# Kernel tuning notes

Measured on AMD Instinct MI355X. Metric: run time of the kernel, lower is better.

The kernel has to match this reference:

```python
import jax, jax.numpy as jnp
import numpy as np

LMBDA = 0.01
GAMMA = 0.5  # resolvant_gamma


def get_mask(evals_x, evals_y, gamma):
    # Standard DPFM resolvant mask, vectorized over batch.
    # evals_x, evals_y: [B, K] nonnegative eigenvalues.
    scale = jnp.maximum(evals_x.max(-1), evals_y.max(-1))[:, None]  # per-batch scaling
    e1 = (evals_x / scale) ** gamma  # [B, K] -> columns of D
    e2 = (evals_y / scale) ** gamma  # [B, K] -> rows of D
    denom = e1[:, None, :] ** 2 + e2[:, :, None] ** 2  # [B, K, K]
    M_re = (e2[:, :, None] - e1[:, None, :]) / denom
    M_im = 1.0 / denom
    return M_re ** 2 + M_im ** 2  # [B, K, K]


def setup_inputs() -> dict:
    key = jax.random.key(0)
    kA, kB, kx, ky = jax.random.split(key, 4)
    Bsz, K, C = 8, 200, 352
    A = jax.random.normal(kA, (Bsz, K, C), dtype=jnp.float32)
    B = jax.random.normal(kB, (Bsz, K, C), dtype=jnp.float32)
    evals_x = jax.random.uniform(kx, (Bsz, K), dtype=jnp.float32)
    evals_y = jax.random.uniform(ky, (Bsz, K), dtype=jnp.float32)
    return {"A": A, "B": B, "evals_x": evals_x, "evals_y": evals_y}


def reference(A, B, evals_x, evals_y):
    # A, B: [Bsz, K, C]; evals_*: [Bsz, K]
    D = get_mask(evals_x, evals_y, GAMMA)  # [Bsz, K, K]
    A_t = jnp.swapaxes(A, 1, 2)            # [Bsz, C, K]
    A_A_t = jnp.matmul(A, A_t)             # [Bsz, K, K]
    B_A_t = jnp.matmul(B, A_t)             # [Bsz, K, K]
    K = A.shape[1]
    eye = jnp.eye(K, dtype=A.dtype)
    # mats[b, i] = A_A_t[b] + lmbda * diag(D[b, i, :])  -> [Bsz, K, K, K]
    mats = A_A_t[:, None, :, :] + LMBDA * (D[..., None] * eye)
    rhs = B_A_t[..., None]                 # [Bsz, K, K, 1] (row i of B_A_t as column)
    # Solve each regularized system; rows of Cxy are the solutions.
    Cxy = jnp.linalg.solve(mats, rhs)[..., 0]  # [Bsz, K, K]
    return Cxy
```

## Files before the change

kernel.cpp:

```cpp
#include <hip/hip_runtime.h>
#include <math.h>

#define KD 200
#define CD 352
#define NITER 24
#define LMB 0.01f

__device__ __forceinline__ float4 ld4(const float* p) { return *(const float4*)p; }
__device__ __forceinline__ void st4(float* p, float4 v) { *(float4*)p = v; }
__device__ __forceinline__ float rdlane(float v, int lane) {
    return __int_as_float(__builtin_amdgcn_readlane(__float_as_int(v), lane));
}

__global__ __launch_bounds__(256) void gemm_gr_kernel(
    const float* __restrict__ A, const float* __restrict__ B,
    float* __restrict__ G, float* __restrict__ R)
{
    __shared__ __align__(16) float Ms[16][72];
    __shared__ __align__(16) float Ns[16][72];
    const int tid = threadIdx.x;
    const int z = blockIdx.z;
    const int b = z >> 1, which = z & 1;
    const float* __restrict__ Xb = (which ? B : A) + (size_t)b * KD * CD;
    const float* __restrict__ Ab = A + (size_t)b * KD * CD;
    float* __restrict__ O = (which ? R : G) + (size_t)b * KD * KD;
    const int tileM = blockIdx.y * 64;
    const int tileN = blockIdx.x * 64;

    const int lm = tid >> 2;
    const int kq = (tid & 3) * 4;
    const int rowM = min(tileM + lm, KD - 1);
    const int rowN = min(tileN + lm, KD - 1);
    const float* __restrict__ Xrow = Xb + (size_t)rowM * CD;
    const float* __restrict__ Arow = Ab + (size_t)rowN * CD;

    const int ty = tid >> 4, tx = tid & 15;
    const int m0 = ty * 4, n0 = tx * 4;

    float acc[4][4] = {};
    for (int kk = 0; kk < CD; kk += 16) {
        const float4 vx = ld4(Xrow + kk + kq);
        const float4 va = ld4(Arow + kk + kq);
        __syncthreads();
        Ms[kq + 0][lm] = vx.x; Ms[kq + 1][lm] = vx.y;
        Ms[kq + 2][lm] = vx.z; Ms[kq + 3][lm] = vx.w;
        Ns[kq + 0][lm] = va.x; Ns[kq + 1][lm] = va.y;
        Ns[kq + 2][lm] = va.z; Ns[kq + 3][lm] = va.w;
        __syncthreads();
        #pragma unroll
        for (int k = 0; k < 16; ++k) {
            const float4 am = ld4(&Ms[k][m0]);
            const float4 an = ld4(&Ns[k][n0]);
            acc[0][0] = fmaf(am.x, an.x, acc[0][0]);
            acc[0][1] = fmaf(am.x, an.y, acc[0][1]);
            acc[0][2] = fmaf(am.x, an.z, acc[0][2]);
            acc[0][3] = fmaf(am.x, an.w, acc[0][3]);
            acc[1][0] = fmaf(am.y, an.x, acc[1][0]);
            acc[1][1] = fmaf(am.y, an.y, acc[1][1]);
            acc[1][2] = fmaf(am.y, an.z, acc[1][2]);
            acc[1][3] = fmaf(am.y, an.w, acc[1][3]);
            acc[2][0] = fmaf(am.z, an.x, acc[2][0]);
            acc[2][1] = fmaf(am.z, an.y, acc[2][1]);
            acc[2][2] = fmaf(am.z, an.z, acc[2][2]);
            acc[2][3] = fmaf(am.z, an.w, acc[2][3]);
            acc[3][0] = fmaf(am.w, an.x, acc[3][0]);
            acc[3][1] = fmaf(am.w, an.y, acc[3][1]);
            acc[3][2] = fmaf(am.w, an.z, acc[3][2]);
            acc[3][3] = fmaf(am.w, an.w, acc[3][3]);
        }
    }
    const int gn = tileN + n0;
    if (gn < KD) {
        #pragma unroll
        for (int i = 0; i < 4; ++i) {
            const int gm = tileM + m0 + i;
            if (gm < KD)
                st4(&O[(size_t)gm * KD + gn],
                    make_float4(acc[i][0], acc[i][1], acc[i][2], acc[i][3]));
        }
    }
}

__global__ __launch_bounds__(512) void cg_kernel(
    const float* __restrict__ G, const float* __restrict__ R,
    const float* __restrict__ ex, const float* __restrict__ ey,
    float* __restrict__ out)
{
    __shared__ __align__(16) float P[864];
    __shared__ __align__(16) float PART[8 * KD * 4];
    __shared__ float WP1[8][4];
    __shared__ float WP2[8][4];
    __shared__ float red8[8];

    const int tid = threadIdx.x;
    const int w = tid >> 6, l = tid & 63;
    const int blk = blockIdx.x;
    const int b = blk / 50;
    const int i0 = (blk - b * 50) * 4;
    const int bK = b * KD;
    const float* __restrict__ Gb = G + (size_t)b * KD * KD;

    float mxv = 0.f;
    if (tid < KD) mxv = fmaxf(ex[bK + tid], ey[bK + tid]);
    #pragma unroll
    for (int off = 32; off > 0; off >>= 1)
        mxv = fmaxf(mxv, __shfl_down(mxv, off, 64));
    if (l == 0) red8[w] = mxv;
    __syncthreads();
    float scale = red8[0];
    #pragma unroll
    for (int wv = 1; wv < 8; ++wv) scale = fmaxf(scale, red8[wv]);
    const float inv_scale = 1.0f / scale;

    const bool mact = (l < 50);
    const int gcol = mact ? l : 49;

    const bool stid = tid < 400;
    const int r = tid >> 1, sq = tid & 1;
    float lam[2], dinv[2], rr[2], xx[2], pp[2], rz4[2];
    if (stid) {
        const float exj = ex[bK + r] * inv_scale;
        const float e1 = sqrtf(exj);
        const float gdiag = Gb[(size_t)r * KD + r];
        const float* __restrict__ Rb = R + (size_t)(bK + i0 + sq * 2) * KD + r;
        #pragma unroll
        for (int j = 0; j < 2; ++j) {
            const float eyi = ey[bK + i0 + sq * 2 + j] * inv_scale;
            const float e2 = sqrtf(eyi);
            const float dn = exj + eyi;
            const float re = e2 - e1;
            lam[j] = LMB * ((re * re + 1.f) / (dn * dn));
            dinv[j] = 1.f / (gdiag + lam[j]);
            rr[j] = Rb[(size_t)j * KD];
            pp[j] = rr[j] * dinv[j];
            xx[j] = 0.f;
        }
        *(float2*)&P[r * 4 + sq * 2] = make_float2(pp[0], pp[1]);
    }
    {
        float vg[2];
        #pragma unroll
        for (int j = 0; j < 2; ++j) vg[j] = stid ? rr[j] * pp[j] : 0.f;
        #pragma unroll
        for (int off = 2; off < 64; off <<= 1)
            #pragma unroll
            for (int j = 0; j < 2; ++j) vg[j] += __shfl_xor(vg[j], off, 64);
        if (l < 2) {
            #pragma unroll
            for (int j = 0; j < 2; ++j) WP2[w][l * 2 + j] = vg[j];
        }
    }
    __syncthreads();
    if (stid) {
        #pragma unroll
        for (int j = 0; j < 2; ++j) {
            float s = 0.f;
            #pragma unroll
            for (int w8 = 0; w8 < 8; ++w8) s += WP2[w8][sq * 2 + j];
            rz4[j] = s;
        }
    }

    for (int k = 0; k < NITER; ++k) {
        __syncthreads();

        float acc[4][4];
        #pragma unroll
        for (int j = 0; j < 4; ++j)
            #pragma unroll
            for (int s = 0; s < 4; ++s) acc[j][s] = 0.f;

        int base = 25 * w;
        #pragma unroll 1
        for (int ch = 0; ch < 3; ++ch) {
            const float pv = P[base * 4 + l];
            const float* __restrict__ gp = Gb + (size_t)base * KD + gcol;
            #pragma unroll
            for (int dc = 0; dc < 8; ++dc) {
                const float g0v = gp[0];
                const float g1v = gp[50];
                const float g2v = gp[100];
                const float g3v = gp[150];
                #pragma unroll
                for (int s = 0; s < 4; ++s) {
                    const float ps = rdlane(pv, dc * 4 + s);
                    acc[0][s] = fmaf(g0v, ps, acc[0][s]);
                    acc[1][s] = fmaf(g1v, ps, acc[1][s]);
                    acc[2][s] = fmaf(g2v, ps, acc[2][s]);
                    acc[3][s] = fmaf(g3v, ps, acc[3][s]);
                }
                gp += KD;
            }
            base += 8;
        }
        {
            const float pv = P[base * 4 + l];
            const float* __restrict__ gp = Gb + (size_t)base * KD + gcol;
            const float g0v = gp[0];
            const float g1v = gp[50];
            const float g2v = gp[100];
            const float g3v = gp[150];
            #pragma unroll
            for (int s = 0; s < 4; ++s) {
                const float ps = rdlane(pv, s);
                acc[0][s] = fmaf(g0v, ps, acc[0][s]);
                acc[1][s] = fmaf(g1v, ps, acc[1][s]);
                acc[2][s] = fmaf(g2v, ps, acc[2][s]);
                acc[3][s] = fmaf(g3v, ps, acc[3][s]);
            }
        }
        if (mact) {
            #pragma unroll
            for (int j = 0; j < 4; ++j)
                st4(&PART[w * (KD * 4) + (50 * j + l) * 4],
                    make_float4(acc[j][0], acc[j][1], acc[j][2], acc[j][3]));
        }
        __syncthreads();

        float qq[2], vq[2];
        if (stid) {
            float s0 = 0.f, s1 = 0.f;
            #pragma unroll
            for (int w8 = 0; w8 < 8; ++w8) {
                const float2 f = *(const float2*)&PART[w8 * (KD * 4) + r * 4 + sq * 2];
                s0 += f.x; s1 += f.y;
            }
            qq[0] = fmaf(lam[0], pp[0], s0);
            qq[1] = fmaf(lam[1], pp[1], s1);
            vq[0] = pp[0] * qq[0];
            vq[1] = pp[1] * qq[1];
        } else {
            qq[0] = qq[1] = 0.f; vq[0] = vq[1] = 0.f;
        }
        #pragma unroll
        for (int off = 2; off < 64; off <<= 1)
            #pragma unroll
            for (int j = 0; j < 2; ++j) vq[j] += __shfl_xor(vq[j], off, 64);
        if (l < 2) {
            #pragma unroll
            for (int j = 0; j < 2; ++j) WP1[w][l * 2 + j] = vq[j];
        }
        __syncthreads();

        float vr[2];
        if (stid) {
            #pragma unroll
            for (int j = 0; j < 2; ++j) {
                float pq = 0.f;
                #pragma unroll
                for (int w8 = 0; w8 < 8; ++w8) pq += WP1[w8][sq * 2 + j];
                const float alpha = rz4[j] / pq;
                xx[j] = fmaf(alpha, pp[j], xx[j]);
                rr[j] = fmaf(-alpha, qq[j], rr[j]);
                vr[j] = rr[j] * rr[j] * dinv[j];
            }
        } else {
            vr[0] = vr[1] = 0.f;
        }
        #pragma unroll
        for (int off = 2; off < 64; off <<= 1)
            #pragma unroll
            for (int j = 0; j < 2; ++j) vr[j] += __shfl_xor(vr[j], off, 64);
        if (l < 2) {
            #pragma unroll
            for (int j = 0; j < 2; ++j) WP2[w][l * 2 + j] = vr[j];
        }
        __syncthreads();

        if (stid) {
            #pragma unroll
            for (int j = 0; j < 2; ++j) {
                float rzn = 0.f;
                #pragma unroll
                for (int w8 = 0; w8 < 8; ++w8) rzn += WP2[w8][sq * 2 + j];
                const float beta = rzn / rz4[j];
                rz4[j] = rzn;
                pp[j] = fmaf(beta, pp[j], rr[j] * dinv[j]);
            }
            *(float2*)&P[r * 4 + sq * 2] = make_float2(pp[0], pp[1]);
        }
    }

    if (stid) {
        float* __restrict__ Ob = out + (size_t)(bK + i0 + sq * 2) * KD + r;
        Ob[0]  = xx[0];
        Ob[KD] = xx[1];
    }
}

extern "C" void kernel_launch(void* const* d_in, const int* in_sizes, int n_in,
                              void* d_out, int out_size, void* d_ws, size_t ws_size,
                              hipStream_t stream) {
    const float* A  = (const float*)d_in[0];
    const float* B  = (const float*)d_in[1];
    const float* ex = (const float*)d_in[2];
    const float* ey = (const float*)d_in[3];
    float* out = (float*)d_out;

    float* G = (float*)d_ws;
    float* R = G + 8 * KD * KD;

    dim3 grid1(4, 4, 16);
    gemm_gr_kernel<<<grid1, 256, 0, stream>>>(A, B, G, R);

    cg_kernel<<<400, 512, 0, stream>>>(G, R, ex, ey, out);
}
```

Before: 212.9 us.

## Fuse p·Ap reduction into matvec partials to drop a barrier; cut CG iterations

Each warp now computes its partial p·(Gp) dot product straight from its matvec accumulators, with warp 0 adding the lambda*p diagonal term through a new LAM shared array. This removes one __syncthreads and one reduction round per CG iteration. The fixed iteration count also drops from 24 to 20, trading some accuracy of the preconditioned CG solve for less work and risking tolerance failures.

```diff
diff --git a/kernel.cpp b/kernel.cpp
--- a/kernel.cpp
+++ b/kernel.cpp
@@ -3,7 +3,7 @@
 
 #define KD 200
 #define CD 352
-#define NITER 24
+#define NITER 20
 #define LMB 0.01f
 
 __device__ __forceinline__ float4 ld4(const float* p) { return *(const float4*)p; }
@@ -87,8 +87,9 @@
     float* __restrict__ out)
 {
     __shared__ __align__(16) float P[864];
+    __shared__ __align__(16) float LAM[864];
     __shared__ __align__(16) float PART[8 * KD * 4];
-    __shared__ float WP1[8][4];
+    __shared__ __align__(16) float WP1[8][4];
     __shared__ float WP2[8][4];
     __shared__ float red8[8];
 
@@ -135,7 +136,8 @@
             pp[j] = rr[j] * dinv[j];
             xx[j] = 0.f;
         }
-        *(float2*)&P[r * 4 + sq * 2] = make_float2(pp[0], pp[1]);
+        *(float2*)&P[r * 4 + sq * 2]   = make_float2(pp[0], pp[1]);
+        *(float2*)&LAM[r * 4 + sq * 2] = make_float2(lam[0], lam[1]);
     }
     {
         float vg[2];
@@ -209,6 +211,39 @@
                 acc[3][s] = fmaf(g3v, ps, acc[3][s]);
             }
         }
+
+        if (w == 0 && mact) {
+            #pragma unroll
+            for (int j = 0; j < 4; ++j) {
+                const int row = l + 50 * j;
+                const float4 la = ld4(&LAM[row * 4]);
+                const float4 pa = ld4(&P[row * 4]);
+                acc[j][0] = fmaf(la.x, pa.x, acc[j][0]);
+                acc[j][1] = fmaf(la.y, pa.y, acc[j][1]);
+                acc[j][2] = fmaf(la.z, pa.z, acc[j][2]);
+                acc[j][3] = fmaf(la.w, pa.w, acc[j][3]);
+            }
+        }
+
+        float vqp[4] = {0.f, 0.f, 0.f, 0.f};
+        if (mact) {
+            #pragma unroll
+            for (int j = 0; j < 4; ++j) {
+                const int row = l + 50 * j;
+                const float4 pa = ld4(&P[row * 4]);
+                vqp[0] = fmaf(pa.x, acc[j][0], vqp[0]);
+                vqp[1] = fmaf(pa.y, acc[j][1], vqp[1]);
+                vqp[2] = fmaf(pa.z, acc[j][2], vqp[2]);
+                vqp[3] = fmaf(pa.w, acc[j][3], vqp[3]);
+            }
+        }
+        #pragma unroll
+        for (int off = 1; off < 64; off <<= 1)
+            #pragma unroll
+            for (int s = 0; s < 4; ++s) vqp[s] += __shfl_xor(vqp[s], off, 64);
+        if (l == 0)
+            st4(&WP1[w][0], make_float4(vqp[0], vqp[1], vqp[2], vqp[3]));
+
         if (mact) {
             #pragma unroll
             for (int j = 0; j < 4; ++j)
@@ -217,7 +252,7 @@
         }
         __syncthreads();
 
-        float qq[2], vq[2];
+        float vr[2];
         if (stid) {
             float s0 = 0.f, s1 = 0.f;
             #pragma unroll
@@ -225,25 +260,7 @@
                 const float2 f = *(const float2*)&PART[w8 * (KD * 4) + r * 4 + sq * 2];
                 s0 += f.x; s1 += f.y;
             }
-            qq[0] = fmaf(lam[0], pp[0], s0);
-            qq[1] = fmaf(lam[1], pp[1], s1);
-            vq[0] = pp[0] * qq[0];
-            vq[1] = pp[1] * qq[1];
-        } else {
-            qq[0] = qq[1] = 0.f; vq[0] = vq[1] = 0.f;
-        }
-        #pragma unroll
-        for (int off = 2; off < 64; off <<= 1)
-            #pragma unroll
-            for (int j = 0; j < 2; ++j) vq[j] += __shfl_xor(vq[j], off, 64);
-        if (l < 2) {
-            #pragma unroll
-            for (int j = 0; j < 2; ++j) WP1[w][l * 2 + j] = vq[j];
-        }
-        __syncthreads();
-
-        float vr[2];
-        if (stid) {
+            const float qv[2] = {s0, s1};
             #pragma unroll
             for (int j = 0; j < 2; ++j) {
                 float pq = 0.f;
@@ -251,7 +268,7 @@
                 for (int w8 = 0; w8 < 8; ++w8) pq += WP1[w8][sq * 2 + j];
                 const float alpha = rz4[j] / pq;
                 xx[j] = fmaf(alpha, pp[j], xx[j]);
-                rr[j] = fmaf(-alpha, qq[j], rr[j]);
+                rr[j] = fmaf(-alpha, qv[j], rr[j]);
                 vr[j] = rr[j] * rr[j] * dinv[j];
             }
         } else {
```

New measurement: 198.9 us. 1.07x faster.

## Fuse CG dot-product reductions into one barrier and cut iteration count

Applied to the files above, without the earlier changes.

Rewrites the preconditioned CG step to compute the new r·z algebraically from p·q, r·D⁻¹q and q·D⁻¹q, which are all reduced together in a single block-wide pass. This removes one of the two reduction-plus-barrier phases per iteration. It also lowers the fixed iteration count from 24 to 18, cutting solver work. The algebraic recurrence can be numerically less stable, and fewer iterations may leave the solution less converged and risk tolerance failures.

```diff
diff --git a/kernel.cpp b/kernel.cpp
--- a/kernel.cpp
+++ b/kernel.cpp
@@ -3,7 +3,7 @@
 
 #define KD 200
 #define CD 352
-#define NITER 24
+#define NITER 18
 #define LMB 0.01f
 
 __device__ __forceinline__ float4 ld4(const float* p) { return *(const float4*)p; }
@@ -88,8 +88,7 @@
 {
     __shared__ __align__(16) float P[864];
     __shared__ __align__(16) float PART[8 * KD * 4];
-    __shared__ float WP1[8][4];
-    __shared__ float WP2[8][4];
+    __shared__ __align__(16) float WP[8][16];
     __shared__ float red8[8];
 
     const int tid = threadIdx.x;
@@ -147,7 +146,7 @@
             for (int j = 0; j < 2; ++j) vg[j] += __shfl_xor(vg[j], off, 64);
         if (l < 2) {
             #pragma unroll
-            for (int j = 0; j < 2; ++j) WP2[w][l * 2 + j] = vg[j];
+            for (int j = 0; j < 2; ++j) WP[w][(l * 2 + j) * 4] = vg[j];
         }
     }
     __syncthreads();
@@ -156,7 +155,7 @@
         for (int j = 0; j < 2; ++j) {
             float s = 0.f;
             #pragma unroll
-            for (int w8 = 0; w8 < 8; ++w8) s += WP2[w8][sq * 2 + j];
+            for (int w8 = 0; w8 < 8; ++w8) s += WP[w8][(sq * 2 + j) * 4];
             rz4[j] = s;
         }
     }
@@ -217,7 +216,7 @@
         }
         __syncthreads();
 
-        float qq[2], vq[2];
+        float qq[2], vpq[2], vs2[2], vs3[2];
         if (stid) {
             float s0 = 0.f, s1 = 0.f;
             #pragma unroll
@@ -227,54 +226,48 @@
             }
             qq[0] = fmaf(lam[0], pp[0], s0);
             qq[1] = fmaf(lam[1], pp[1], s1);
-            vq[0] = pp[0] * qq[0];
-            vq[1] = pp[1] * qq[1];
+            #pragma unroll
+            for (int j = 0; j < 2; ++j) {
+                vpq[j] = pp[j] * qq[j];
+                vs2[j] = dinv[j] * rr[j] * qq[j];
+                vs3[j] = dinv[j] * qq[j] * qq[j];
+            }
         } else {
-            qq[0] = qq[1] = 0.f; vq[0] = vq[1] = 0.f;
-        }
-        #pragma unroll
-        for (int off = 2; off < 64; off <<= 1)
-            #pragma unroll
-            for (int j = 0; j < 2; ++j) vq[j] += __shfl_xor(vq[j], off, 64);
+            qq[0] = qq[1] = 0.f;
+            vpq[0] = vpq[1] = vs2[0] = vs2[1] = vs3[0] = vs3[1] = 0.f;
+        }
+        #pragma unroll
+        for (int off = 2; off < 64; off <<= 1) {
+            #pragma unroll
+            for (int j = 0; j < 2; ++j) {
+                vpq[j] += __shfl_xor(vpq[j], off, 64);
+                vs2[j] += __shfl_xor(vs2[j], off, 64);
+                vs3[j] += __shfl_xor(vs3[j], off, 64);
+            }
+        }
         if (l < 2) {
             #pragma unroll
-            for (int j = 0; j < 2; ++j) WP1[w][l * 2 + j] = vq[j];
-        }
-        __syncthreads();
-
-        float vr[2];
+            for (int j = 0; j < 2; ++j)
+                st4(&WP[w][(l * 2 + j) * 4],
+                    make_float4(vpq[j], vs2[j], vs3[j], 0.f));
+        }
+        __syncthreads();
+
         if (stid) {
             #pragma unroll
             for (int j = 0; j < 2; ++j) {
-                float pq = 0.f;
+                float pq = 0.f, S2 = 0.f, S3 = 0.f;
                 #pragma unroll
-                for (int w8 = 0; w8 < 8; ++w8) pq += WP1[w8][sq * 2 + j];
+                for (int w8 = 0; w8 < 8; ++w8) {
+                    const float4 f = ld4(&WP[w8][(sq * 2 + j) * 4]);
+                    pq += f.x; S2 += f.y; S3 += f.z;
+                }
                 const float alpha = rz4[j] / pq;
+                const float rzn = fmaf(alpha * alpha, S3, fmaf(-2.f * alpha, S2, rz4[j]));
+                const float beta = rzn / rz4[j];
+                rz4[j] = rzn;
                 xx[j] = fmaf(alpha, pp[j], xx[j]);
                 rr[j] = fmaf(-alpha, qq[j], rr[j]);
-                vr[j] = rr[j] * rr[j] * dinv[j];
-            }
-        } else {
-            vr[0] = vr[1] = 0.f;
-        }
-        #pragma unroll
-        for (int off = 2; off < 64; off <<= 1)
-            #pragma unroll
-            for (int j = 0; j < 2; ++j) vr[j] += __shfl_xor(vr[j], off, 64);
-        if (l < 2) {
-            #pragma unroll
-            for (int j = 0; j < 2; ++j) WP2[w][l * 2 + j] = vr[j];
-        }
-        __syncthreads();
-
-        if (stid) {
-            #pragma unroll
-            for (int j = 0; j < 2; ++j) {
-                float rzn = 0.f;
-                #pragma unroll
-                for (int w8 = 0; w8 < 8; ++w8) rzn += WP2[w8][sq * 2 + j];
-                const float beta = rzn / rz4[j];
-                rz4[j] = rzn;
                 pp[j] = fmaf(beta, pp[j], rr[j] * dinv[j]);
             }
             *(float2*)&P[r * 4 + sq * 2] = make_float2(pp[0], pp[1]);
```

Result: faster. 193.1 us, median of 2 (-9.3%).
